# Optimization experiments

Hardware: AMD Instinct MI355X
Metric: run time of the kernel (lower is better)

The kernel has to match this reference:

```python
import jax, jax.numpy as jnp
import numpy as np

B, P, H = 32768, 128, 64

def setup_inputs() -> dict:
    key = jax.random.key(0)
    ks = jax.random.split(key, 6)
    planet_xy = jax.random.normal(ks[0], (B, P, 2), dtype=jnp.float32)
    planet_m = jax.random.uniform(ks[1], (P,), dtype=jnp.float32)
    ast_xy = jax.random.normal(ks[2], (B, 2), dtype=jnp.float32)
    W1 = jax.random.normal(ks[3], (4, H), dtype=jnp.float32) * 0.5
    b1 = jnp.zeros((H,), dtype=jnp.float32)
    W2 = jax.random.normal(ks[4], (H, H), dtype=jnp.float32) * 0.125
    b2 = jnp.zeros((H,), dtype=jnp.float32)
    return {"planet_xy": planet_xy, "planet_m": planet_m, "ast_xy": ast_xy,
            "W1": W1, "b1": b1, "W2": W2, "b2": b2}

def reference(planet_xy, planet_m, ast_xy, W1, b1, W2, b2):
    # d: (B, P, 2) broadcast difference planet - asteroid
    d = planet_xy - ast_xy[:, None, :]
    dist2 = jnp.sum(d * d, axis=-1) + 1e-6            # (B, P)
    invdist = 1.0 / jnp.sqrt(dist2)                   # (B, P)
    m = jnp.broadcast_to(planet_m[None, :], dist2.shape)  # (B, P)
    feats = jnp.concatenate([d, invdist[..., None], m[..., None]], axis=-1)  # (B, P, 4)
    h = jax.nn.relu(jnp.einsum('bpf,fh->bph', feats, W1) + b1)  # (B, P, H)
    msg = jax.nn.relu(jnp.einsum('bph,hk->bpk', h, W2) + b2)    # (B, P, H)
    return msg.sum(axis=1)                             # (B, H)
```

## Files before the change

### kernel.cpp

```cpp
#include <hip/hip_runtime.h>
#include <hip/hip_fp16.h>

#define NP    128
#define NH    64
#define ITERS 4
#define WPB   4

typedef __attribute__((ext_vector_type(8))) _Float16 f16x8;
typedef __attribute__((ext_vector_type(4))) _Float16 f16x4;
typedef __attribute__((ext_vector_type(2))) __fp16  hf16x2;
typedef __attribute__((ext_vector_type(4))) float f32x4;

union FragK16 { f16x4 v; unsigned int u[2]; };
union FragK32 { f16x8 v; unsigned int u[4]; };

__device__ __forceinline__ unsigned int pack_pkrtz(float a, float b) {
    hf16x2 t = __builtin_amdgcn_cvt_pkrtz(a, b);
    return __builtin_bit_cast(unsigned int, t);
}

__device__ __forceinline__ unsigned int relu2_pk(unsigned int u) {
    hf16x2 h = __builtin_bit_cast(hf16x2, u);
    h = __builtin_elementwise_max(h, (hf16x2)(__fp16)0.f);
    return __builtin_bit_cast(unsigned int, h);
}

__global__ void __launch_bounds__(256, 2) gnn_wave(
    const float* __restrict__ planet_xy,
    const float* __restrict__ planet_m,
    const float* __restrict__ ast_xy,
    const float* __restrict__ W1,
    const float* __restrict__ b1,
    const float* __restrict__ W2,
    const float* __restrict__ b2,
    float* __restrict__ out)
{
    const int tid  = threadIdx.x;
    const int wv   = tid >> 6;
    const int lane = tid & 63;
    const int q    = lane >> 4;
    const int lm   = lane & 15;
    const bool q0  = (q == 0);
    const bool q1  = (q == 1);

    FragK16 w1f[4];
    #pragma unroll
    for (int mt = 0; mt < 4; mt++) {
        const int m = 16 * mt + lm;
        float wa = W1[0 * NH + m], wb = W1[1 * NH + m];
        float wc = W1[2 * NH + m], wd = W1[3 * NH + m];
        float be = b1[m];
        w1f[mt].u[0] = q0 ? pack_pkrtz(wa, wb) : (q1 ? pack_pkrtz(be, 0.f) : 0u);
        w1f[mt].u[1] = q0 ? pack_pkrtz(wc, wd) : 0u;
    }

    FragK32 w2b[4][2];
    #pragma unroll
    for (int np = 0; np < 4; np++)
        #pragma unroll
        for (int kk = 0; kk < 2; kk++) {
            const int n = 16 * np + lm;
            const int k0 = 32 * kk + 4 * q;
            const int k1 = 32 * kk + 16 + 4 * q;
            w2b[np][kk].u[0] = pack_pkrtz(W2[(k0 + 0) * NH + n], W2[(k0 + 1) * NH + n]);
            w2b[np][kk].u[1] = pack_pkrtz(W2[(k0 + 2) * NH + n], W2[(k0 + 3) * NH + n]);
            w2b[np][kk].u[2] = pack_pkrtz(W2[(k1 + 0) * NH + n], W2[(k1 + 1) * NH + n]);
            w2b[np][kk].u[3] = pack_pkrtz(W2[(k1 + 2) * NH + n], W2[(k1 + 3) * NH + n]);
        }

    f32x4 b2f[4];
    #pragma unroll
    for (int np = 0; np < 4; np++) {
        const float bv = b2[16 * np + lm];
        b2f[np] = (f32x4){bv, bv, bv, bv};
    }

    float pmv[8];
    #pragma unroll
    for (int i = 0; i < 8; i++)
        pmv[i] = planet_m[16 * i + lm];

    const unsigned int bf0_const = q1 ? pack_pkrtz(1.f, 0.f) : 0u;
    const f32x4 zf = (f32x4){0.f, 0.f, 0.f, 0.f};

    FragK16 onesA;
    onesA.u[0] = 0x3C003C00u;
    onesA.u[1] = 0x3C003C00u;

    int b = (blockIdx.x * WPB + wv) * ITERS;

    float2 axy = *(const float2*)&ast_xy[2 * b];
    float2 pxy[8];
    #pragma unroll
    for (int i = 0; i < 8; i++)
        pxy[i] = *(const float2*)&planet_xy[((size_t)b * NP + 16 * i + lm) * 2];

    #pragma unroll 1
    for (int it = 0; it < ITERS; ++it, ++b) {
        const int bn = (it + 1 < ITERS) ? b + 1 : b;
        const float* pnext = planet_xy + ((size_t)bn * NP + lm) * 2;

        float2 axN = axy;

        f32x4 redD[4];
        #pragma unroll
        for (int np = 0; np < 4; np++)
            redD[np] = zf;

        f32x4 c[4];
        {
            float dx = pxy[0].x - axy.x, dy = pxy[0].y - axy.y;
            float inv = __builtin_amdgcn_rsqf(fmaf(dx, dx, fmaf(dy, dy, 1e-6f)));
            FragK16 bf;
            bf.u[0] = q0 ? pack_pkrtz(dx, dy)       : bf0_const;
            bf.u[1] = q0 ? pack_pkrtz(inv, pmv[0])  : 0u;
            #pragma unroll
            for (int mt = 0; mt < 4; mt++)
                c[mt] = __builtin_amdgcn_mfma_f32_16x16x16f16(w1f[mt].v, bf.v, zf, 0, 0, 0);
        }

        #pragma unroll
        for (int mi = 0; mi < 8; ++mi) {
            FragK32 hA[2];
            #pragma unroll
            for (int mt = 0; mt < 4; mt++) {
                hA[mt >> 1].u[2 * (mt & 1) + 0] = relu2_pk(pack_pkrtz(c[mt][0], c[mt][1]));
                hA[mt >> 1].u[2 * (mt & 1) + 1] = relu2_pk(pack_pkrtz(c[mt][2], c[mt][3]));
            }

            if (mi < 7) {
                float dx = pxy[mi + 1].x - axy.x, dy = pxy[mi + 1].y - axy.y;
                float inv = __builtin_amdgcn_rsqf(fmaf(dx, dx, fmaf(dy, dy, 1e-6f)));
                FragK16 bf;
                bf.u[0] = q0 ? pack_pkrtz(dx, dy)            : bf0_const;
                bf.u[1] = q0 ? pack_pkrtz(inv, pmv[mi + 1])  : 0u;
                #pragma unroll
                for (int mt = 0; mt < 4; mt++)
                    c[mt] = __builtin_amdgcn_mfma_f32_16x16x16f16(w1f[mt].v, bf.v, zf, 0, 0, 0);
            }

            pxy[mi] = *(const float2*)(pnext + 32 * mi);
            if (mi == 5)
                axN = *(const float2*)&ast_xy[2 * bn];

            f32x4 acc[4];
            #pragma unroll
            for (int np = 0; np < 4; np++)
                acc[np] = __builtin_amdgcn_mfma_f32_16x16x32_f16(hA[0].v, w2b[np][0].v, b2f[np], 0, 0, 0);
            #pragma unroll
            for (int np = 0; np < 4; np++)
                acc[np] = __builtin_amdgcn_mfma_f32_16x16x32_f16(hA[1].v, w2b[np][1].v, acc[np], 0, 0, 0);

            FragK16 mf[4];
            #pragma unroll
            for (int np = 0; np < 4; np++) {
                mf[np].u[0] = relu2_pk(pack_pkrtz(acc[np][0], acc[np][1]));
                mf[np].u[1] = relu2_pk(pack_pkrtz(acc[np][2], acc[np][3]));
            }
            #pragma unroll
            for (int np = 0; np < 4; np++)
                redD[np] = __builtin_amdgcn_mfma_f32_16x16x16f16(onesA.v, mf[np].v, redD[np], 0, 0, 0);
        }

        axy = axN;

        float v = q0 ? redD[0][0]
                : q1 ? redD[1][0]
                : (q == 2) ? redD[2][0] : redD[3][0];
        out[(size_t)b * NH + lane] = v;
    }
}

extern "C" void kernel_launch(void* const* d_in, const int* in_sizes, int n_in,
                              void* d_out, int out_size, void* d_ws, size_t ws_size,
                              hipStream_t stream) {
    const float* planet_xy = (const float*)d_in[0];
    const float* planet_m  = (const float*)d_in[1];
    const float* ast_xy    = (const float*)d_in[2];
    const float* W1        = (const float*)d_in[3];
    const float* b1        = (const float*)d_in[4];
    const float* W2        = (const float*)d_in[5];
    const float* b2        = (const float*)d_in[6];
    float* outp            = (float*)d_out;

    const int B = in_sizes[2] / 2;
    const int batches_per_block = WPB * ITERS;
    const int grid = (B + batches_per_block - 1) / batches_per_block;

    gnn_wave<<<grid, 256, 0, stream>>>(planet_xy, planet_m, ast_xy, W1, b1, W2, b2, outp);
}
```

Measured before the change: 123.6 us.

## Interleave two batch elements per wave to hide MFMA dependency latency

Replaces the software-pipelined single-batch loop, which computed the next layer-1 chunk while running layer-2 on the current one and prefetched the next batch's planets, with a loop that processes two batch elements at once. Independent MFMA chains for A and B are interleaved so each can hide the other's latency. Each pair's planet data is now loaded at the top of its iteration with no prefetch, which may expose global-load latency and raises register pressure under the 2-blocks-per-CU launch bound.

```diff
diff --git a/kernel.cpp b/kernel.cpp
--- a/kernel.cpp
+++ b/kernel.cpp
@@ -3,7 +3,7 @@
 
 #define NP    128
 #define NH    64
-#define ITERS 4
+#define PAIRS 2
 #define WPB   4
 
 typedef __attribute__((ext_vector_type(8))) _Float16 f16x8;
@@ -87,87 +87,111 @@
     onesA.u[0] = 0x3C003C00u;
     onesA.u[1] = 0x3C003C00u;
 
-    int b = (blockIdx.x * WPB + wv) * ITERS;
-
-    float2 axy = *(const float2*)&ast_xy[2 * b];
-    float2 pxy[8];
-    #pragma unroll
-    for (int i = 0; i < 8; i++)
-        pxy[i] = *(const float2*)&planet_xy[((size_t)b * NP + 16 * i + lm) * 2];
+    int b = (blockIdx.x * WPB + wv) * (2 * PAIRS);
 
     #pragma unroll 1
-    for (int it = 0; it < ITERS; ++it, ++b) {
-        const int bn = (it + 1 < ITERS) ? b + 1 : b;
-        const float* pnext = planet_xy + ((size_t)bn * NP + lm) * 2;
-
-        float2 axN = axy;
-
-        f32x4 redD[4];
-        #pragma unroll
-        for (int np = 0; np < 4; np++)
-            redD[np] = zf;
-
-        f32x4 c[4];
-        {
-            float dx = pxy[0].x - axy.x, dy = pxy[0].y - axy.y;
-            float inv = __builtin_amdgcn_rsqf(fmaf(dx, dx, fmaf(dy, dy, 1e-6f)));
-            FragK16 bf;
-            bf.u[0] = q0 ? pack_pkrtz(dx, dy)       : bf0_const;
-            bf.u[1] = q0 ? pack_pkrtz(inv, pmv[0])  : 0u;
-            #pragma unroll
-            for (int mt = 0; mt < 4; mt++)
-                c[mt] = __builtin_amdgcn_mfma_f32_16x16x16f16(w1f[mt].v, bf.v, zf, 0, 0, 0);
+    for (int pr = 0; pr < PAIRS; ++pr, b += 2) {
+        const int bA = b, bB = b + 1;
+
+        const float2 axA = *(const float2*)&ast_xy[2 * bA];
+        const float2 axB = *(const float2*)&ast_xy[2 * bB];
+        float2 pxA[8], pxB[8];
+        #pragma unroll
+        for (int i = 0; i < 8; i++) {
+            pxA[i] = *(const float2*)&planet_xy[((size_t)bA * NP + 16 * i + lm) * 2];
+            pxB[i] = *(const float2*)&planet_xy[((size_t)bB * NP + 16 * i + lm) * 2];
         }
 
+        f32x4 rdA[4], rdB[4];
+        #pragma unroll
+        for (int np = 0; np < 4; np++) { rdA[np] = zf; rdB[np] = zf; }
+
         #pragma unroll
         for (int mi = 0; mi < 8; ++mi) {
-            FragK32 hA[2];
-            #pragma unroll
-            for (int mt = 0; mt < 4; mt++) {
-                hA[mt >> 1].u[2 * (mt & 1) + 0] = relu2_pk(pack_pkrtz(c[mt][0], c[mt][1]));
-                hA[mt >> 1].u[2 * (mt & 1) + 1] = relu2_pk(pack_pkrtz(c[mt][2], c[mt][3]));
-            }
-
-            if (mi < 7) {
-                float dx = pxy[mi + 1].x - axy.x, dy = pxy[mi + 1].y - axy.y;
+            f32x4 cA[4], cB[4];
+            {
+                float dx = pxA[mi].x - axA.x, dy = pxA[mi].y - axA.y;
                 float inv = __builtin_amdgcn_rsqf(fmaf(dx, dx, fmaf(dy, dy, 1e-6f)));
                 FragK16 bf;
-                bf.u[0] = q0 ? pack_pkrtz(dx, dy)            : bf0_const;
-                bf.u[1] = q0 ? pack_pkrtz(inv, pmv[mi + 1])  : 0u;
+                bf.u[0] = q0 ? pack_pkrtz(dx, dy)        : bf0_const;
+                bf.u[1] = q0 ? pack_pkrtz(inv, pmv[mi])  : 0u;
                 #pragma unroll
                 for (int mt = 0; mt < 4; mt++)
-                    c[mt] = __builtin_amdgcn_mfma_f32_16x16x16f16(w1f[mt].v, bf.v, zf, 0, 0, 0);
-            }
-
-            pxy[mi] = *(const float2*)(pnext + 32 * mi);
-            if (mi == 5)
-                axN = *(const float2*)&ast_xy[2 * bn];
-
-            f32x4 acc[4];
-            #pragma unroll
-            for (int np = 0; np < 4; np++)
-                acc[np] = __builtin_amdgcn_mfma_f32_16x16x32_f16(hA[0].v, w2b[np][0].v, b2f[np], 0, 0, 0);
-            #pragma unroll
-            for (int np = 0; np < 4; np++)
-                acc[np] = __builtin_amdgcn_mfma_f32_16x16x32_f16(hA[1].v, w2b[np][1].v, acc[np], 0, 0, 0);
-
-            FragK16 mf[4];
-            #pragma unroll
-            for (int np = 0; np < 4; np++) {
-                mf[np].u[0] = relu2_pk(pack_pkrtz(acc[np][0], acc[np][1]));
-                mf[np].u[1] = relu2_pk(pack_pkrtz(acc[np][2], acc[np][3]));
-            }
-            #pragma unroll
-            for (int np = 0; np < 4; np++)
-                redD[np] = __builtin_amdgcn_mfma_f32_16x16x16f16(onesA.v, mf[np].v, redD[np], 0, 0, 0);
+                    cA[mt] = __builtin_amdgcn_mfma_f32_16x16x16f16(w1f[mt].v, bf.v, zf, 0, 0, 0);
+            }
+            {
+                float dx = pxB[mi].x - axB.x, dy = pxB[mi].y - axB.y;
+                float inv = __builtin_amdgcn_rsqf(fmaf(dx, dx, fmaf(dy, dy, 1e-6f)));
+                FragK16 bf;
+                bf.u[0] = q0 ? pack_pkrtz(dx, dy)        : bf0_const;
+                bf.u[1] = q0 ? pack_pkrtz(inv, pmv[mi])  : 0u;
+                #pragma unroll
+                for (int mt = 0; mt < 4; mt++)
+                    cB[mt] = __builtin_amdgcn_mfma_f32_16x16x16f16(w1f[mt].v, bf.v, zf, 0, 0, 0);
+            }
+
+            f32x4 accA[4], accB[4];
+            {
+                FragK32 hA[2];
+                #pragma unroll
+                for (int mt = 0; mt < 4; mt++) {
+                    hA[mt >> 1].u[2 * (mt & 1) + 0] = relu2_pk(pack_pkrtz(cA[mt][0], cA[mt][1]));
+                    hA[mt >> 1].u[2 * (mt & 1) + 1] = relu2_pk(pack_pkrtz(cA[mt][2], cA[mt][3]));
+                }
+                #pragma unroll
+                for (int np = 0; np < 4; np++)
+                    accA[np] = __builtin_amdgcn_mfma_f32_16x16x32_f16(hA[0].v, w2b[np][0].v, b2f[np], 0, 0, 0);
+                #pragma unroll
+                for (int np = 0; np < 4; np++)
+                    accA[np] = __builtin_amdgcn_mfma_f32_16x16x32_f16(hA[1].v, w2b[np][1].v, accA[np], 0, 0, 0);
+            }
+            {
+                FragK32 hB[2];
+                #pragma unroll
+                for (int mt = 0; mt < 4; mt++) {
+                    hB[mt >> 1].u[2 * (mt & 1) + 0] = relu2_pk(pack_pkrtz(cB[mt][0], cB[mt][1]));
+                    hB[mt >> 1].u[2 * (mt & 1) + 1] = relu2_pk(pack_pkrtz(cB[mt][2], cB[mt][3]));
+                }
+                #pragma unroll
+                for (int np = 0; np < 4; np++)
+                    accB[np] = __builtin_amdgcn_mfma_f32_16x16x32_f16(hB[0].v, w2b[np][0].v, b2f[np], 0, 0, 0);
+                #pragma unroll
+                for (int np = 0; np < 4; np++)
+                    accB[np] = __builtin_amdgcn_mfma_f32_16x16x32_f16(hB[1].v, w2b[np][1].v, accB[np], 0, 0, 0);
+            }
+
+            {
+                FragK16 mf[4];
+                #pragma unroll
+                for (int np = 0; np < 4; np++) {
+                    mf[np].u[0] = relu2_pk(pack_pkrtz(accA[np][0], accA[np][1]));
+                    mf[np].u[1] = relu2_pk(pack_pkrtz(accA[np][2], accA[np][3]));
+                }
+                #pragma unroll
+                for (int np = 0; np < 4; np++)
+                    rdA[np] = __builtin_amdgcn_mfma_f32_16x16x16f16(onesA.v, mf[np].v, rdA[np], 0, 0, 0);
+            }
+            {
+                FragK16 mf[4];
+                #pragma unroll
+                for (int np = 0; np < 4; np++) {
+                    mf[np].u[0] = relu2_pk(pack_pkrtz(accB[np][0], accB[np][1]));
+                    mf[np].u[1] = relu2_pk(pack_pkrtz(accB[np][2], accB[np][3]));
+                }
+                #pragma unroll
+                for (int np = 0; np < 4; np++)
+                    rdB[np] = __builtin_amdgcn_mfma_f32_16x16x16f16(onesA.v, mf[np].v, rdB[np], 0, 0, 0);
+            }
         }
 
-        axy = axN;
-
-        float v = q0 ? redD[0][0]
-                : q1 ? redD[1][0]
-                : (q == 2) ? redD[2][0] : redD[3][0];
-        out[(size_t)b * NH + lane] = v;
+        float vA = q0 ? rdA[0][0]
+                 : q1 ? rdA[1][0]
+                 : (q == 2) ? rdA[2][0] : rdA[3][0];
+        float vB = q0 ? rdB[0][0]
+                 : q1 ? rdB[1][0]
+                 : (q == 2) ? rdB[2][0] : rdB[3][0];
+        out[(size_t)bA * NH + lane] = vA;
+        out[(size_t)bB * NH + lane] = vB;
     }
 }
 
@@ -184,7 +208,7 @@
     float* outp            = (float*)d_out;
 
     const int B = in_sizes[2] / 2;
-    const int batches_per_block = WPB * ITERS;
+    const int batches_per_block = WPB * 2 * PAIRS;
     const int grid = (B + batches_per_block - 1) / batches_per_block;
 
     gnn_wave<<<grid, 256, 0, stream>>>(planet_xy, planet_m, ast_xy, W1, b1, W2, b2, outp);
```

Result: slower. 128.0 us (+3.6%).
